# Kernel tuning notes

Hardware: AMD Instinct MI355X
Metric: run time of the kernel (lower is better)

The kernel has to match this reference:

```python
import jax, jax.numpy as jnp
import numpy as np

N = 50000
E = 800000
D = 128


def _gcn_layer(x, row, col, ew, W, b, n):
    # PyG GCNConv (normalize=True, add_self_loops=True):
    # self-loops were already appended to row/col/ew by the caller.
    deg = jax.ops.segment_sum(ew, col, num_segments=n)          # [N]
    dis = jnp.where(deg > 0, jax.lax.rsqrt(jnp.maximum(deg, 1e-12)), 0.0)
    norm = dis[row] * ew * dis[col]                              # [E+N]
    h = x @ W                                                    # [N, D]
    msg = h[row] * norm[:, None]                                 # [E+N, D] gather-scale
    out = jax.ops.segment_sum(msg, col, num_segments=n)          # scatter-add
    return out + b


def setup_inputs() -> dict:
    key = jax.random.key(0)
    k1, k2, k3, k4, k5 = jax.random.split(key, 5)
    x = jax.random.normal(k1, (N, D), dtype=jnp.float32)
    edge_index = jax.random.randint(k2, (2, E), 0, N, dtype=jnp.int64)
    edge_weight = jax.random.uniform(k3, (E,), dtype=jnp.float32)
    s = 1.0 / np.sqrt(D)
    W1 = jax.random.uniform(k4, (D, D), minval=-s, maxval=s, dtype=jnp.float32)
    b1 = jnp.zeros((D,), dtype=jnp.float32)
    W2 = jax.random.uniform(k5, (D, D), minval=-s, maxval=s, dtype=jnp.float32)
    b2 = jnp.zeros((D,), dtype=jnp.float32)
    return {"x": x, "edge_index": edge_index, "edge_weight": edge_weight,
            "W1": W1, "b1": b1, "W2": W2, "b2": b2}


def reference(x, edge_index, edge_weight, W1, b1, W2, b2):
    n = x.shape[0]
    loop = jnp.arange(n, dtype=edge_index.dtype)
    row = jnp.concatenate([edge_index[0], loop])
    col = jnp.concatenate([edge_index[1], loop])
    ew = jnp.concatenate([edge_weight, jnp.ones((n,), dtype=edge_weight.dtype)])
    h = _gcn_layer(x, row, col, ew, W1, b1, n)
    h = jax.nn.relu(h)
    # F.dropout(training=self.training): identity in eval mode
    out = _gcn_layer(h, row, col, ew, W2, b2, n)
    return out
```

## Files before the change

### kernel.cpp

```cpp
#include <hip/hip_runtime.h>

#define NN 50000
#define NE 800000
#define DD 128

#define FIX_SCALE 16777216.0f
#define NWELEM 16384
#define GEMM_GRID ((NN + 127) / 128)

#define SHIFT2 7
#define BWID 128
#define NBUCK ((NN + BWID - 1) / BWID)
#define CAP2 2560
#define NB1 500
#define EPB (NE / NB1)
#define EQ4 (EPB / 4)
#define NBK_PAD 392

typedef __attribute__((ext_vector_type(8))) short short8;
typedef __attribute__((ext_vector_type(4))) float floatx4;
typedef __attribute__((ext_vector_type(2))) _Float16 half2v;
typedef __attribute__((ext_vector_type(4))) _Float16 half4;
typedef __attribute__((ext_vector_type(8))) _Float16 half8;


__device__ __forceinline__ void split_trunc(float x, short& hi, short& lo) {
    unsigned uh = __float_as_uint(x) >> 16;
    hi = (short)uh;
    float r = x - __uint_as_float(uh << 16);
    lo = (short)(__float_as_uint(r) >> 16);
}


__global__ __launch_bounds__(256) void init_hist(const int* __restrict__ col,
                                                 unsigned* __restrict__ hist,
                                                 const float* __restrict__ W1, const float* __restrict__ W2,
                                                 unsigned short* __restrict__ w1hi, unsigned short* __restrict__ w1lo,
                                                 unsigned short* __restrict__ w2hi, unsigned short* __restrict__ w2lo) {
    if (blockIdx.x < NB1) {
        __shared__ unsigned h[NBUCK];
        for (int k = threadIdx.x; k < NBUCK; k += 256) h[k] = 0u;
        __syncthreads();
        const int4* c4p = (const int4*)(col + blockIdx.x * EPB);
#pragma unroll
        for (int it = 0; it < 2; it++) {
            int q = it * 256 + (int)threadIdx.x;
            if (q < EQ4) {
                int4 c4 = c4p[q];
                atomicAdd(&h[c4.x >> SHIFT2], 1u);
                atomicAdd(&h[c4.y >> SHIFT2], 1u);
                atomicAdd(&h[c4.z >> SHIFT2], 1u);
                atomicAdd(&h[c4.w >> SHIFT2], 1u);
            }
        }
        __syncthreads();
        unsigned* hb = hist + (size_t)blockIdx.x * NBK_PAD;
        for (int k = threadIdx.x; k < NBUCK; k += 256) hb[k] = h[k];
    } else {
        int u = (blockIdx.x - NB1) * 256 + threadIdx.x;
        int which = u >> 14;
        int idx = u & (NWELEM - 1);
        int k = idx >> 7, n = idx & 127;
        const float* W = which ? W2 : W1;
        unsigned short* whi = which ? w2hi : w1hi;
        unsigned short* wlo = which ? w2lo : w1lo;
        short h, l;
        split_trunc(W[idx], h, l);
        whi[n * DD + k] = (unsigned short)h;
        wlo[n * DD + k] = (unsigned short)l;
    }
}


__global__ __launch_bounds__(512) void bucket_prefix(const unsigned* __restrict__ hist,
                                                     unsigned* __restrict__ offs_t,
                                                     unsigned* __restrict__ bcur) {
    __shared__ unsigned sa[512], sb[512];
    int k = blockIdx.x;
    int t = threadIdx.x;
    unsigned v = (t < NB1) ? hist[(size_t)t * NBK_PAD + k] : 0u;
    sa[t] = v;
    __syncthreads();
    unsigned* src = sa;
    unsigned* dst = sb;
    for (int d = 1; d < 512; d <<= 1) {
        unsigned x = src[t] + (t >= d ? src[t - d] : 0u);
        dst[t] = x;
        __syncthreads();
        unsigned* tmp = src; src = dst; dst = tmp;
    }
    unsigned inc = src[t];
    if (t < NB1) offs_t[(size_t)t * NBK_PAD + k] = inc - v;
    if (t == 511) bcur[k] = inc;
}


template <bool RELU, bool SCALE, typename InT>
__device__ __forceinline__ void gemm_core(int bid, const InT* __restrict__ in,
                                          const unsigned short* __restrict__ whi,
                                          const unsigned short* __restrict__ wlo,
                                          const float* __restrict__ dis,
                                          _Float16* __restrict__ out) {
    int lane = threadIdx.x & 63;
    int wid = threadIdx.x >> 6;
    int cg = wid & 1;
    int rg = wid >> 1;
    int l16 = lane & 15;
    int quad = lane >> 4;
    int koff_base = quad * 8;

    short8 bhi[4][4], blo[4][4];
#pragma unroll
    for (int t = 0; t < 4; t++) {
        int n = cg * 64 + t * 16 + l16;
#pragma unroll
        for (int ks = 0; ks < 4; ks++) {
            int koff = ks * 32 + koff_base;
            bhi[t][ks] = *(const short8*)(whi + n * DD + koff);
            blo[t][ks] = *(const short8*)(wlo + n * DD + koff);
        }
    }

#pragma unroll
    for (int chunk = 0; chunk < 4; chunk++) {
        int base = bid * 128 + chunk * 32 + rg * 16;
        int m = base + l16;
        int mld = (m < NN) ? m : 0;
        const InT* xr = in + (size_t)mld * DD;

        short8 ahi[4], alo[4];
#pragma unroll
        for (int ks = 0; ks < 4; ks++) {
            int koff = ks * 32 + koff_base;
            float v[8];
            if constexpr (sizeof(InT) == 4) {
                float4 a0 = *(const float4*)(xr + koff);
                float4 a1 = *(const float4*)(xr + koff + 4);
                v[0] = a0.x; v[1] = a0.y; v[2] = a0.z; v[3] = a0.w;
                v[4] = a1.x; v[5] = a1.y; v[6] = a1.z; v[7] = a1.w;
            } else {
                half8 a = *(const half8*)(xr + koff);
#pragma unroll
                for (int j = 0; j < 8; j++) v[j] = (float)a[j];
            }
#pragma unroll
            for (int j = 0; j < 8; j++) {
                float xv = RELU ? fmaxf(v[j], 0.0f) : v[j];
                short h, l;
                split_trunc(xv, h, l);
                ahi[ks][j] = h;
                alo[ks][j] = l;
            }
        }

        floatx4 acc[4];
#pragma unroll
        for (int t = 0; t < 4; t++) acc[t] = (floatx4)(0.0f);

#pragma unroll
        for (int ks = 0; ks < 4; ks++) {
#pragma unroll
            for (int t = 0; t < 4; t++) {
                acc[t] = __builtin_amdgcn_mfma_f32_16x16x32_bf16(ahi[ks], bhi[t][ks], acc[t], 0, 0, 0);
                acc[t] = __builtin_amdgcn_mfma_f32_16x16x32_bf16(alo[ks], bhi[t][ks], acc[t], 0, 0, 0);
                acc[t] = __builtin_amdgcn_mfma_f32_16x16x32_bf16(ahi[ks], blo[t][ks], acc[t], 0, 0, 0);
            }
        }

#pragma unroll
        for (int r = 0; r < 4; r++) {
            int rowm = base + quad * 4 + r;
            if (rowm < NN) {
                float dsc = SCALE ? dis[rowm] : 1.0f;
                _Float16* o = out + (size_t)rowm * DD + cg * 64 + l16;
#pragma unroll
                for (int t = 0; t < 4; t++) o[t * 16] = (_Float16)(acc[t][r] * dsc);
            }
        }
    }
}


__device__ __forceinline__ void scatter_core(int bid, const int* __restrict__ row,
                                             const int* __restrict__ col,
                                             const float* __restrict__ ew,
                                             const unsigned* __restrict__ offs_t,
                                             uint2* __restrict__ staged) {
    __shared__ unsigned base1[NBUCK];
    __shared__ unsigned cnt1[NBUCK];

    const unsigned* ob = offs_t + (size_t)bid * NBK_PAD;
    for (int k = threadIdx.x; k < NBUCK; k += 256) {
        base1[k] = (unsigned)k * CAP2 + ob[k];
        cnt1[k] = 0u;
    }
    __syncthreads();

    int e0 = bid * EPB;
    const int4* c4p = (const int4*)(col + e0);
    const int4* r4p = (const int4*)(row + e0);
    const float4* w4p = (const float4*)(ew + e0);

#pragma unroll
    for (int it = 0; it < 2; it++) {
        int q = it * 256 + (int)threadIdx.x;
        if (q < EQ4) {
            int4 c4 = c4p[q];
            int4 r4 = r4p[q];
            float4 w4 = w4p[q];
            int cc[4] = {c4.x, c4.y, c4.z, c4.w};
            int rr[4] = {r4.x, r4.y, r4.z, r4.w};
            float wv[4] = {w4.x, w4.y, w4.z, w4.w};
#pragma unroll
            for (int j = 0; j < 4; j++) {
                int bk = cc[j] >> SHIFT2;
                unsigned r = base1[bk] + atomicAdd(&cnt1[bk], 1u);
                unsigned lim = (unsigned)bk * CAP2 + (CAP2 - 1);
                if (r > lim) r = lim;
                uint2 p;
                p.x = (unsigned)rr[j] | ((unsigned)(cc[j] & (BWID - 1)) << 16);
                p.y = __float_as_uint(wv[j]);
                staged[r] = p;
            }
        }
    }
}


__global__ __launch_bounds__(256) void gemm1_scatter(const float* __restrict__ x,
                                                     const unsigned short* __restrict__ w1hi,
                                                     const unsigned short* __restrict__ w1lo,
                                                     _Float16* __restrict__ g,
                                                     const int* __restrict__ row,
                                                     const int* __restrict__ col,
                                                     const float* __restrict__ ew,
                                                     const unsigned* __restrict__ offs_t,
                                                     uint2* __restrict__ staged) {
    if (blockIdx.x < NB1) {
        scatter_core(blockIdx.x, row, col, ew, offs_t, staged);
    } else {
        gemm_core<false, false, float>(blockIdx.x - NB1, x, w1hi, w1lo, nullptr, g);
    }
}

__global__ __launch_bounds__(256, 2) void gemm2(const _Float16* __restrict__ in,
                                                const unsigned short* __restrict__ whi,
                                                const unsigned short* __restrict__ wlo,
                                                const float* __restrict__ dis,
                                                _Float16* __restrict__ out) {
    gemm_core<true, true, _Float16>(blockIdx.x, in, whi, wlo, dis, out);
}


__global__ __launch_bounds__(256) void bucket_dis(const unsigned* __restrict__ bcur,
                                                  const uint2* __restrict__ staged,
                                                  float* __restrict__ dis,
                                                  _Float16* __restrict__ g) {
    __shared__ unsigned wfix[BWID];
    __shared__ float disS[BWID];

    int b = blockIdx.x;
    int node0 = b << SHIFT2;
    int nn = min(BWID, NN - node0);

    if (threadIdx.x < BWID) wfix[threadIdx.x] = 0u;
    __syncthreads();

    int m = min((int)bcur[b], CAP2);
    const uint2* st = staged + (size_t)b * CAP2;

    for (int j = threadIdx.x; j < m; j += 256) {
        uint2 p = st[j];
        int ln = p.x >> 16;
        float w = __uint_as_float(p.y);
        atomicAdd(&wfix[ln], (unsigned)(w * FIX_SCALE + 0.5f));
    }
    __syncthreads();

    if (threadIdx.x < (unsigned)nn) {
        float deg = 1.0f + (float)wfix[threadIdx.x] * (1.0f / FIX_SCALE);
        float d = rsqrtf(deg);
        disS[threadIdx.x] = d;
        dis[node0 + threadIdx.x] = d;
    }
    __syncthreads();

    half8* gb = (half8*)(g + (size_t)node0 * DD);
    for (int idx = threadIdx.x; idx < nn * 16; idx += 256) {
        float d = disS[idx >> 4];
        half8 hv = gb[idx];
#pragma unroll
        for (int jj = 0; jj < 8; jj++) hv[jj] = (_Float16)((float)hv[jj] * d);
        gb[idx] = hv;
    }
}


template <typename OutT>
__global__ __launch_bounds__(1024) void agg_sorted(const unsigned* __restrict__ bcur,
                                                   const uint2* __restrict__ staged,
                                                   const _Float16* __restrict__ g,
                                                   const float* __restrict__ dis,
                                                   const float* __restrict__ bias,
                                                   OutT* __restrict__ out) {
    __shared__ uint2 sRAW[CAP2];
    __shared__ uint2 sED[CAP2];
    __shared__ unsigned cnt[BWID];
    __shared__ unsigned cur[BWID];
    __shared__ unsigned off[BWID];
    __shared__ unsigned sc[BWID];

    int b = blockIdx.x;
    int node0 = b << SHIFT2;
    int nn = min(BWID, NN - node0);

    if (threadIdx.x < BWID) cnt[threadIdx.x] = 0u;
    __syncthreads();

    int m = min((int)bcur[b], CAP2);
    const uint2* st = staged + (size_t)b * CAP2;

    for (int j = threadIdx.x; j < m; j += 1024) {
        uint2 p = st[j];
        sRAW[j] = p;
        atomicAdd(&cnt[p.x >> 16], 1u);
    }
    __syncthreads();

    if (threadIdx.x < BWID) sc[threadIdx.x] = cnt[threadIdx.x];
    __syncthreads();
    for (int d = 1; d < BWID; d <<= 1) {
        unsigned v = 0;
        if (threadIdx.x < BWID) {
            v = sc[threadIdx.x];
            if ((int)threadIdx.x >= d) v += sc[threadIdx.x - d];
        }
        __syncthreads();
        if (threadIdx.x < BWID) sc[threadIdx.x] = v;
        __syncthreads();
    }
    if (threadIdx.x < BWID) {
        off[threadIdx.x] = sc[threadIdx.x] - cnt[threadIdx.x];
        cur[threadIdx.x] = 0u;
    }
    __syncthreads();

    for (int j = threadIdx.x; j < m; j += 1024) {
        uint2 p = sRAW[j];
        int ln = p.x >> 16;
        unsigned r = off[ln] + atomicAdd(&cur[ln], 1u);
        uint2 q;
        q.x = (p.x & 0xFFFFu) << 7;
        q.y = p.y;
        sED[r] = q;
    }
    __syncthreads();

    int wid = threadIdx.x >> 6;
    int lane = threadIdx.x & 63;
    for (int ln = wid; ln < nn; ln += 16) {
        int s0 = (int)off[ln];
        int e0 = s0 + (int)cnt[ln];
        float a0 = 0.0f, a1 = 0.0f;
        int j = s0;
        for (; j + 3 < e0; j += 4) {
            uint2 p0 = sED[j], p1 = sED[j + 1], p2 = sED[j + 2], p3 = sED[j + 3];
            half2v v0 = *(const half2v*)(g + p0.x + 2 * lane);
            half2v v1 = *(const half2v*)(g + p1.x + 2 * lane);
            half2v v2 = *(const half2v*)(g + p2.x + 2 * lane);
            half2v v3 = *(const half2v*)(g + p3.x + 2 * lane);
            float w0 = __uint_as_float(p0.y), w1 = __uint_as_float(p1.y);
            float w2 = __uint_as_float(p2.y), w3 = __uint_as_float(p3.y);
            a0 = fmaf(w0, (float)v0.x, a0); a1 = fmaf(w0, (float)v0.y, a1);
            a0 = fmaf(w1, (float)v1.x, a0); a1 = fmaf(w1, (float)v1.y, a1);
            a0 = fmaf(w2, (float)v2.x, a0); a1 = fmaf(w2, (float)v2.y, a1);
            a0 = fmaf(w3, (float)v3.x, a0); a1 = fmaf(w3, (float)v3.y, a1);
        }
        for (; j < e0; ++j) {
            uint2 p0 = sED[j];
            half2v v0 = *(const half2v*)(g + p0.x + 2 * lane);
            float w0 = __uint_as_float(p0.y);
            a0 = fmaf(w0, (float)v0.x, a0); a1 = fmaf(w0, (float)v0.y, a1);
        }
        int i = node0 + ln;
        float d = dis[i];
        half2v gs = *(const half2v*)(g + (size_t)i * DD + 2 * lane);
        float2 bb = *(const float2*)(bias + 2 * lane);
        float o0 = bb.x + d * (a0 + (float)gs.x);
        float o1 = bb.y + d * (a1 + (float)gs.y);
        if constexpr (sizeof(OutT) == 2) {
            half2v o; o.x = (_Float16)o0; o.y = (_Float16)o1;
            *(half2v*)(out + (size_t)i * DD + 2 * lane) = o;
        } else {
            float2 o; o.x = o0; o.y = o1;
            *(float2*)(out + (size_t)i * DD + 2 * lane) = o;
        }
    }
}


extern "C" void kernel_launch(void* const* d_in, const int* in_sizes, int n_in,
                              void* d_out, int out_size, void* d_ws, size_t ws_size,
                              hipStream_t stream) {
    const float* x  = (const float*)d_in[0];
    const int*   ei = (const int*)d_in[1];
    const float* ew = (const float*)d_in[2];
    const float* W1 = (const float*)d_in[3];
    const float* b1 = (const float*)d_in[4];
    const float* W2 = (const float*)d_in[5];
    const float* b2 = (const float*)d_in[6];
    float* out = (float*)d_out;

    float* ws      = (float*)d_ws;
    float* dis     = ws;
    unsigned* bcur = (unsigned*)(ws + 50000);
    unsigned* hist = (unsigned*)(ws + 150000);
    unsigned* offs_t = (unsigned*)(ws + 400000);
    uint2* staged  = (uint2*)(ws + 900000);
    _Float16* gbuf = (_Float16*)(ws + 7300000);
    unsigned short* wt1hi = (unsigned short*)(ws + 10500000);
    unsigned short* wt1lo = (unsigned short*)(ws + 10508192);
    unsigned short* wt2hi = (unsigned short*)(ws + 10516384);
    unsigned short* wt2lo = (unsigned short*)(ws + 10524576);
    _Float16* out1 = (_Float16*)(ws + 10532768);

    const int* rowi = ei;
    const int* coli = ei + NE;

    init_hist<<<NB1 + (2 * NWELEM) / 256, 256, 0, stream>>>(
        coli, hist, W1, W2, wt1hi, wt1lo, wt2hi, wt2lo);

    bucket_prefix<<<NBUCK, 512, 0, stream>>>(hist, offs_t, bcur);

    gemm1_scatter<<<NB1 + GEMM_GRID, 256, 0, stream>>>(
        x, wt1hi, wt1lo, gbuf, rowi, coli, ew, offs_t, staged);

    bucket_dis<<<NBUCK, 256, 0, stream>>>(bcur, staged, dis, gbuf);

    agg_sorted<_Float16><<<NBUCK, 1024, 0, stream>>>(bcur, staged, gbuf, dis, b1, out1);

    gemm2<<<GEMM_GRID, 256, 0, stream>>>(out1, wt2hi, wt2lo, dis, gbuf);

    agg_sorted<float><<<NBUCK, 1024, 0, stream>>>(bcur, staged, gbuf, dis, b2, out);
}
```

Baseline: 213.4 us.

## Sort bucket edges once and reuse sorted CSR in both aggregation passes

The per-bucket counting sort, previously done twice inside each aggregation kernel, moves into the degree/normalization kernel. That kernel packs the count and fixed-point weight sum into one 64-bit shared atomic and writes the sorted edge list plus per-node offset/count to global memory. The aggregation kernels then load only their slice of the pre-sorted edges, use half-bucket blocks of 512 threads for twice as many blocks, and unroll the gather by 8. This removes the duplicated sort and its barriers, at the cost of an extra global write/read of the sorted edges and a cap of HCAP edges per half bucket, which can silently truncate edges.

```diff
diff --git a/kernel.cpp b/kernel.cpp
--- a/kernel.cpp
+++ b/kernel.cpp
@@ -5,6 +5,7 @@
 #define DD 128
 
 #define FIX_SCALE 16777216.0f
+#define LOW40 ((1ULL << 40) - 1)
 #define NWELEM 16384
 #define GEMM_GRID ((NN + 127) / 128)
 
@@ -16,11 +17,11 @@
 #define EPB (NE / NB1)
 #define EQ4 (EPB / 4)
 #define NBK_PAD 392
+#define HCAP 1536
 
 typedef __attribute__((ext_vector_type(8))) short short8;
 typedef __attribute__((ext_vector_type(4))) float floatx4;
 typedef __attribute__((ext_vector_type(2))) _Float16 half2v;
-typedef __attribute__((ext_vector_type(4))) _Float16 half4;
 typedef __attribute__((ext_vector_type(8))) _Float16 half8;
 
 
@@ -252,117 +253,150 @@
 }
 
 
-__global__ __launch_bounds__(256) void bucket_dis(const unsigned* __restrict__ bcur,
-                                                  const uint2* __restrict__ staged,
-                                                  float* __restrict__ dis,
-                                                  _Float16* __restrict__ g) {
-    __shared__ unsigned wfix[BWID];
+__global__ __launch_bounds__(512) void bucket_sortdis(const unsigned* __restrict__ bcur,
+                                                      const uint2* __restrict__ staged,
+                                                      uint2* __restrict__ sorted,
+                                                      unsigned* __restrict__ offcnt,
+                                                      float* __restrict__ dis,
+                                                      _Float16* __restrict__ g) {
+    __shared__ uint2 sRAW[CAP2];
+    __shared__ uint2 sED[CAP2];
+    __shared__ unsigned long long wcnt[BWID];
+    __shared__ unsigned sc[BWID];
+    __shared__ unsigned offs[BWID];
+    __shared__ unsigned cur[BWID];
     __shared__ float disS[BWID];
 
     int b = blockIdx.x;
     int node0 = b << SHIFT2;
     int nn = min(BWID, NN - node0);
-
-    if (threadIdx.x < BWID) wfix[threadIdx.x] = 0u;
+    int t = threadIdx.x;
+
+    if (t < BWID) { wcnt[t] = 0ULL; cur[t] = 0u; }
     __syncthreads();
 
     int m = min((int)bcur[b], CAP2);
     const uint2* st = staged + (size_t)b * CAP2;
 
-    for (int j = threadIdx.x; j < m; j += 256) {
+    for (int j = t; j < m; j += 512) {
         uint2 p = st[j];
+        sRAW[j] = p;
         int ln = p.x >> 16;
         float w = __uint_as_float(p.y);
-        atomicAdd(&wfix[ln], (unsigned)(w * FIX_SCALE + 0.5f));
-    }
-    __syncthreads();
-
-    if (threadIdx.x < (unsigned)nn) {
-        float deg = 1.0f + (float)wfix[threadIdx.x] * (1.0f / FIX_SCALE);
-        float d = rsqrtf(deg);
-        disS[threadIdx.x] = d;
-        dis[node0 + threadIdx.x] = d;
-    }
-    __syncthreads();
-
-    half8* gb = (half8*)(g + (size_t)node0 * DD);
-    for (int idx = threadIdx.x; idx < nn * 16; idx += 256) {
-        float d = disS[idx >> 4];
-        half8 hv = gb[idx];
-#pragma unroll
-        for (int jj = 0; jj < 8; jj++) hv[jj] = (_Float16)((float)hv[jj] * d);
-        gb[idx] = hv;
-    }
-}
-
-
-template <typename OutT>
-__global__ __launch_bounds__(1024) void agg_sorted(const unsigned* __restrict__ bcur,
-                                                   const uint2* __restrict__ staged,
-                                                   const _Float16* __restrict__ g,
-                                                   const float* __restrict__ dis,
-                                                   const float* __restrict__ bias,
-                                                   OutT* __restrict__ out) {
-    __shared__ uint2 sRAW[CAP2];
-    __shared__ uint2 sED[CAP2];
-    __shared__ unsigned cnt[BWID];
-    __shared__ unsigned cur[BWID];
-    __shared__ unsigned off[BWID];
-    __shared__ unsigned sc[BWID];
-
-    int b = blockIdx.x;
-    int node0 = b << SHIFT2;
-    int nn = min(BWID, NN - node0);
-
-    if (threadIdx.x < BWID) cnt[threadIdx.x] = 0u;
-    __syncthreads();
-
-    int m = min((int)bcur[b], CAP2);
-    const uint2* st = staged + (size_t)b * CAP2;
-
-    for (int j = threadIdx.x; j < m; j += 1024) {
-        uint2 p = st[j];
-        sRAW[j] = p;
-        atomicAdd(&cnt[p.x >> 16], 1u);
-    }
-    __syncthreads();
-
-    if (threadIdx.x < BWID) sc[threadIdx.x] = cnt[threadIdx.x];
+        unsigned q = (unsigned)(w * FIX_SCALE + 0.5f);
+        atomicAdd(&wcnt[ln], (1ULL << 40) | (unsigned long long)q);
+    }
+    __syncthreads();
+
+    if (t < BWID) sc[t] = (unsigned)(wcnt[t] >> 40);
     __syncthreads();
     for (int d = 1; d < BWID; d <<= 1) {
         unsigned v = 0;
-        if (threadIdx.x < BWID) {
-            v = sc[threadIdx.x];
-            if ((int)threadIdx.x >= d) v += sc[threadIdx.x - d];
-        }
+        if (t < BWID) { v = sc[t]; if (t >= d) v += sc[t - d]; }
         __syncthreads();
-        if (threadIdx.x < BWID) sc[threadIdx.x] = v;
+        if (t < BWID) sc[t] = v;
         __syncthreads();
     }
-    if (threadIdx.x < BWID) {
-        off[threadIdx.x] = sc[threadIdx.x] - cnt[threadIdx.x];
-        cur[threadIdx.x] = 0u;
-    }
-    __syncthreads();
-
-    for (int j = threadIdx.x; j < m; j += 1024) {
+    if (t < BWID) {
+        unsigned long long cv = wcnt[t];
+        unsigned c = (unsigned)(cv >> 40);
+        unsigned off = sc[t] - c;
+        offs[t] = off;
+        if (t < (unsigned)nn) {
+            int i = node0 + t;
+            float deg = 1.0f + (float)(cv & LOW40) * (1.0f / FIX_SCALE);
+            float d = rsqrtf(deg);
+            disS[t] = d;
+            dis[i] = d;
+            offcnt[i] = (off << 16) | c;
+        }
+    }
+    __syncthreads();
+
+    for (int j = t; j < m; j += 512) {
         uint2 p = sRAW[j];
         int ln = p.x >> 16;
-        unsigned r = off[ln] + atomicAdd(&cur[ln], 1u);
+        unsigned r = offs[ln] + atomicAdd(&cur[ln], 1u);
         uint2 q;
         q.x = (p.x & 0xFFFFu) << 7;
         q.y = p.y;
         sED[r] = q;
     }
     __syncthreads();
+    uint2* dst = sorted + (size_t)b * CAP2;
+    int m2 = (m + 1) >> 1;
+    for (int j = t; j < m2; j += 512) ((uint4*)dst)[j] = ((const uint4*)sED)[j];
+
+    half8* gb = (half8*)(g + (size_t)node0 * DD);
+    for (int idx = t; idx < nn * 16; idx += 512) {
+        float d = disS[idx >> 4];
+        half8 hv = gb[idx];
+#pragma unroll
+        for (int jj = 0; jj < 8; jj++) hv[jj] = (_Float16)((float)hv[jj] * d);
+        gb[idx] = hv;
+    }
+}
+
+
+template <typename OutT>
+__global__ __launch_bounds__(512) void agg_gather(const uint2* __restrict__ sorted,
+                                                  const unsigned* __restrict__ offcnt,
+                                                  const _Float16* __restrict__ g,
+                                                  const float* __restrict__ dis,
+                                                  const float* __restrict__ bias,
+                                                  OutT* __restrict__ out) {
+    __shared__ uint2 sED[HCAP];
+
+    int hb = blockIdx.x;
+    int b = hb >> 1;
+    int half = hb & 1;
+    int node0 = (b << SHIFT2) + half * 64;
+    int nloc = min(64, NN - node0);
+
+    unsigned ocf = offcnt[node0];
+    unsigned ocl = offcnt[node0 + nloc - 1];
+    int first = (int)(ocf >> 16);
+    int end = (int)(ocl >> 16) + (int)(ocl & 0xFFFFu);
+    int mloc = min(end - first, HCAP);
+
+    const uint2* st = sorted + (size_t)b * CAP2 + first;
+    for (int j = threadIdx.x; j < mloc; j += 512) sED[j] = st[j];
+    __syncthreads();
 
     int wid = threadIdx.x >> 6;
     int lane = threadIdx.x & 63;
-    for (int ln = wid; ln < nn; ln += 16) {
-        int s0 = (int)off[ln];
-        int e0 = s0 + (int)cnt[ln];
+
+    for (int ln = wid; ln < nloc; ln += 8) {
+        int i = node0 + ln;
+        unsigned oc = offcnt[i];
+        int s0 = (int)(oc >> 16) - first;
+        int e0 = min(s0 + (int)(oc & 0xFFFFu), mloc);
         float a0 = 0.0f, a1 = 0.0f;
         int j = s0;
+        for (; j + 7 < e0; j += 8) {
+            uint2 p0 = sED[j],     p1 = sED[j + 1], p2 = sED[j + 2], p3 = sED[j + 3];
+            uint2 p4 = sED[j + 4], p5 = sED[j + 5], p6 = sED[j + 6], p7 = sED[j + 7];
+            half2v v0 = *(const half2v*)(g + p0.x + 2 * lane);
+            half2v v1 = *(const half2v*)(g + p1.x + 2 * lane);
+            half2v v2 = *(const half2v*)(g + p2.x + 2 * lane);
+            half2v v3 = *(const half2v*)(g + p3.x + 2 * lane);
+            half2v v4 = *(const half2v*)(g + p4.x + 2 * lane);
+            half2v v5 = *(const half2v*)(g + p5.x + 2 * lane);
+            half2v v6 = *(const half2v*)(g + p6.x + 2 * lane);
+            half2v v7 = *(const half2v*)(g + p7.x + 2 * lane);
+            float w0 = __uint_as_float(p0.y), w1 = __uint_as_float(p1.y);
+            float w2 = __uint_as_float(p2.y), w3 = __uint_as_float(p3.y);
+            float w4 = __uint_as_float(p4.y), w5 = __uint_as_float(p5.y);
+            float w6 = __uint_as_float(p6.y), w7 = __uint_as_float(p7.y);
+            a0 = fmaf(w0, (float)v0.x, a0); a1 = fmaf(w0, (float)v0.y, a1);
+            a0 = fmaf(w1, (float)v1.x, a0); a1 = fmaf(w1, (float)v1.y, a1);
+            a0 = fmaf(w2, (float)v2.x, a0); a1 = fmaf(w2, (float)v2.y, a1);
+            a0 = fmaf(w3, (float)v3.x, a0); a1 = fmaf(w3, (float)v3.y, a1);
+            a0 = fmaf(w4, (float)v4.x, a0); a1 = fmaf(w4, (float)v4.y, a1);
+            a0 = fmaf(w5, (float)v5.x, a0); a1 = fmaf(w5, (float)v5.y, a1);
+            a0 = fmaf(w6, (float)v6.x, a0); a1 = fmaf(w6, (float)v6.y, a1);
+            a0 = fmaf(w7, (float)v7.x, a0); a1 = fmaf(w7, (float)v7.y, a1);
+        }
         for (; j + 3 < e0; j += 4) {
             uint2 p0 = sED[j], p1 = sED[j + 1], p2 = sED[j + 2], p3 = sED[j + 3];
             half2v v0 = *(const half2v*)(g + p0.x + 2 * lane);
@@ -382,7 +416,6 @@
             float w0 = __uint_as_float(p0.y);
             a0 = fmaf(w0, (float)v0.x, a0); a1 = fmaf(w0, (float)v0.y, a1);
         }
-        int i = node0 + ln;
         float d = dis[i];
         half2v gs = *(const half2v*)(g + (size_t)i * DD + 2 * lane);
         float2 bb = *(const float2*)(bias + 2 * lane);
@@ -414,9 +447,11 @@
     float* ws      = (float*)d_ws;
     float* dis     = ws;
     unsigned* bcur = (unsigned*)(ws + 50000);
+    unsigned* offcnt = (unsigned*)(ws + 100000);
     unsigned* hist = (unsigned*)(ws + 150000);
     unsigned* offs_t = (unsigned*)(ws + 400000);
     uint2* staged  = (uint2*)(ws + 900000);
+    uint2* sorted  = (uint2*)(ws + 3000000);
     _Float16* gbuf = (_Float16*)(ws + 7300000);
     unsigned short* wt1hi = (unsigned short*)(ws + 10500000);
     unsigned short* wt1lo = (unsigned short*)(ws + 10508192);
@@ -435,11 +470,13 @@
     gemm1_scatter<<<NB1 + GEMM_GRID, 256, 0, stream>>>(
         x, wt1hi, wt1lo, gbuf, rowi, coli, ew, offs_t, staged);
 
-    bucket_dis<<<NBUCK, 256, 0, stream>>>(bcur, staged, dis, gbuf);
-
-    agg_sorted<_Float16><<<NBUCK, 1024, 0, stream>>>(bcur, staged, gbuf, dis, b1, out1);
+    bucket_sortdis<<<NBUCK, 512, 0, stream>>>(bcur, staged, sorted, offcnt, dis, gbuf);
+
+    const int agg_grid = 2 * NBUCK;
+
+    agg_gather<_Float16><<<agg_grid, 512, 0, stream>>>(sorted, offcnt, gbuf, dis, b1, out1);
 
     gemm2<<<GEMM_GRID, 256, 0, stream>>>(out1, wt2hi, wt2lo, dis, gbuf);
 
-    agg_sorted<float><<<NBUCK, 1024, 0, stream>>>(bcur, staged, gbuf, dis, b2, out);
-}
+    agg_gather<float><<<agg_grid, 512, 0, stream>>>(sorted, offcnt, gbuf, dis, b2, out);
+}
```

Result: no change. 214.0 us (+0.3%).
